# Performance work log

Hardware: AMD Instinct MI355X
Metric: run time of the kernel (lower is better)

## Reference

```python
import jax, jax.numpy as jnp
import numpy as np

N_NODES = 100000
N_EDGES = 1600000
N_FEAT = 128
HIDDEN = 64
N_CLASSES = 40


def setup_inputs() -> dict:
    key = jax.random.key(0)
    ks = jax.random.split(key, 4)
    x = jax.random.normal(ks[0], (N_NODES, N_FEAT), dtype=jnp.float32)
    edge_index = jax.random.randint(ks[1], (2, N_EDGES), 0, N_NODES, dtype=jnp.int64)
    # Glorot-style init like PyG GCNConv
    W1 = jax.random.normal(ks[2], (N_FEAT, HIDDEN), dtype=jnp.float32) * (1.0 / np.sqrt(N_FEAT))
    b1 = jnp.zeros((HIDDEN,), dtype=jnp.float32)
    W2 = jax.random.normal(ks[3], (HIDDEN, N_CLASSES), dtype=jnp.float32) * (1.0 / np.sqrt(HIDDEN))
    b2 = jnp.zeros((N_CLASSES,), dtype=jnp.float32)
    return {"x": x, "edge_index": edge_index, "W1": W1, "b1": b1, "W2": W2, "b2": b2}


def _gcn_conv(x, src, dst, norm, W, b, n_nodes):
    # PyG GCNConv: transform first, then normalized scatter-add aggregation
    h = x @ W                                   # [N, out]
    msg = h[src] * norm[:, None]                # [E+N, out] gather
    out = jax.ops.segment_sum(msg, dst, num_segments=n_nodes)  # scatter-add
    return out + b


def _norm_and_loops(edge_index, n_nodes):
    # add self-loops, symmetric normalization deg^{-1/2} A_hat deg^{-1/2}
    loop = jnp.arange(n_nodes, dtype=edge_index.dtype)
    src = jnp.concatenate([edge_index[0], loop])
    dst = jnp.concatenate([edge_index[1], loop])
    deg = jax.ops.segment_sum(jnp.ones_like(dst, dtype=jnp.float32), dst, num_segments=n_nodes)
    dinv = jnp.where(deg > 0, jax.lax.rsqrt(jnp.maximum(deg, 1.0)), 0.0)
    norm = dinv[src] * dinv[dst]
    return src, dst, norm


def reference(x, edge_index, W1, b1, W2, b2):
    n_nodes = x.shape[0]
    src, dst, norm = _norm_and_loops(edge_index, n_nodes)
    h = _gcn_conv(x, src, dst, norm, W1, b1, n_nodes)
    h = jax.nn.relu(h)
    h = _gcn_conv(h, src, dst, norm, W2, b2, n_nodes)
    return jax.nn.log_softmax(h, axis=1)
```

## Files before the change

### kernel.cpp

```cpp
#include <hip/hip_runtime.h>
#include <hip/hip_bf16.h>
#include <string.h>

#define N_FEAT 128
#define HIDDEN 64
#define N_CLS  40
#define EDGE_BLOCKS 1024
#define PLACE_BLOCKS 1024
#define PLACE_CHUNK 8192

typedef __bf16 bf16x8 __attribute__((ext_vector_type(8)));
typedef float  f32x4  __attribute__((ext_vector_type(4)));

union Frag { unsigned u[4]; bf16x8 v; };

static __device__ inline int get_xcc() {
    return (int)(__builtin_amdgcn_s_getreg((3 << 11) | 20) & 7u);
}


static __device__ inline unsigned pack_bf16(float a, float b) {
    unsigned ba = __float_as_uint(a);
    unsigned bb = __float_as_uint(b);
    unsigned ra = (ba + 0x7fffu + ((ba >> 16) & 1u)) >> 16;
    unsigned rb = (bb + 0x7fffu + ((bb >> 16) & 1u)) >> 16;
    return (ra & 0xffffu) | (rb << 16);
}

static __device__ inline float2 unpack_bf16(unsigned v) {
    return make_float2(__uint_as_float(v << 16), __uint_as_float(v & 0xffff0000u));
}


__global__ void detect_layout_kernel(const int* __restrict__ ei, int* __restrict__ flag) {
    int lane = threadIdx.x;
    int v = ei[2 * lane + 1];
    unsigned long long b = __ballot(v != 0);
    if (lane == 0) flag[0] = (b == 0ull) ? 1 : 0;
}


__global__ __launch_bounds__(256) void count_deg_kernel(const int* __restrict__ ei,
                                                        const int* __restrict__ flag,
                                                        unsigned* __restrict__ deg, int E) {
    bool is64 = (flag[0] != 0);
    int idx = blockIdx.x * 256 + threadIdx.x;
    if (is64) {
        int Eeven = E & ~1;
        int stride2 = gridDim.x * 256 * 2;
        for (int e = idx * 2; e < Eeven; e += stride2) {
            uint4 dv = *(const uint4*)(ei + (size_t)2 * E + (size_t)2 * e);
            atomicAdd(&deg[(int)dv.x], 1u);
            atomicAdd(&deg[(int)dv.z], 1u);
        }
        for (int e = Eeven + idx; e < E; e += gridDim.x * 256)
            atomicAdd(&deg[ei[(size_t)2 * E + (size_t)2 * e]], 1u);
    } else {
        for (int e = idx; e < E; e += gridDim.x * 256)
            atomicAdd(&deg[ei[(size_t)E + e]], 1u);
    }
}


__global__ __launch_bounds__(256) void scan_local_kernel(const unsigned* __restrict__ deg,
                                                         unsigned* __restrict__ rowptr,
                                                         float* __restrict__ dinv,
                                                         unsigned* __restrict__ partial, int N) {
    __shared__ unsigned tmp[256];
    int i = blockIdx.x * 256 + threadIdx.x;
    unsigned v = (i < N) ? deg[i] : 0u;
    if (i < N) dinv[i] = rsqrtf((float)(v + 1u));
    tmp[threadIdx.x] = v;
    __syncthreads();
#pragma unroll
    for (int off = 1; off < 256; off <<= 1) {
        unsigned t = (threadIdx.x >= (unsigned)off) ? tmp[threadIdx.x - off] : 0u;
        __syncthreads();
        tmp[threadIdx.x] += t;
        __syncthreads();
    }
    if (i < N) rowptr[i] = tmp[threadIdx.x] - v;
    if (threadIdx.x == 255) partial[blockIdx.x] = tmp[255];
}

__global__ __launch_bounds__(512) void scan_partial_kernel(unsigned* __restrict__ partial, int npart) {
    __shared__ unsigned tmp[512];
    unsigned v = ((int)threadIdx.x < npart) ? partial[threadIdx.x] : 0u;
    tmp[threadIdx.x] = v;
    __syncthreads();
#pragma unroll
    for (int off = 1; off < 512; off <<= 1) {
        unsigned t = (threadIdx.x >= (unsigned)off) ? tmp[threadIdx.x - off] : 0u;
        __syncthreads();
        tmp[threadIdx.x] += t;
        __syncthreads();
    }
    if ((int)threadIdx.x < npart) partial[threadIdx.x] = tmp[threadIdx.x] - v;
}

__global__ __launch_bounds__(256) void scan_add_kernel(unsigned* __restrict__ rowptr,
                                                       const unsigned* __restrict__ partial,
                                                       unsigned* __restrict__ cur, int N) {
    int i = blockIdx.x * 256 + threadIdx.x;
    if (i < N) {
        unsigned r = rowptr[i] + partial[blockIdx.x];
        rowptr[i] = r;
        cur[i] = r;
    }
}


__global__ __launch_bounds__(256) void place_xcd_kernel(const int* __restrict__ ei,
                                                        const int* __restrict__ flag,
                                                        unsigned* __restrict__ cur,
                                                        unsigned* __restrict__ ctr,
                                                        int* __restrict__ csr_src,
                                                        int E, int N) {
    int r = get_xcc();
    int npx = (N + 7) >> 3;
    int nlo = r * npx;
    int nhi = min(N, nlo + npx);
    bool is64 = (flag[0] != 0);
    __shared__ unsigned chunk_s;
    for (;;) {
        if (threadIdx.x == 0)
            chunk_s = __hip_atomic_fetch_add(&ctr[r * 64], 1u, __ATOMIC_RELAXED,
                                             __HIP_MEMORY_SCOPE_WORKGROUP);
        __syncthreads();
        long long base = (long long)chunk_s * PLACE_CHUNK;
        __syncthreads();
        if (base >= E) break;
        int end = (int)min((long long)E, base + PLACE_CHUNK);
        if (is64) {
            for (int e = (int)base + 2 * threadIdx.x; e + 1 < end; e += 512) {
                uint4 sv = *(const uint4*)(ei + (size_t)2 * e);
                uint4 dv = *(const uint4*)(ei + (size_t)2 * E + (size_t)2 * e);
                int d0 = (int)dv.x, d1 = (int)dv.z;
                if (d0 >= nlo && d0 < nhi) {
                    unsigned p = atomicAdd(&cur[d0], 1u);
                    csr_src[p] = (int)sv.x;
                }
                if (d1 >= nlo && d1 < nhi) {
                    unsigned p = atomicAdd(&cur[d1], 1u);
                    csr_src[p] = (int)sv.z;
                }
            }
            if ((end - (int)base) & 1) {
                if (threadIdx.x == 0) {
                    int e = end - 1;
                    int d = ei[(size_t)2 * E + (size_t)2 * e];
                    if (d >= nlo && d < nhi) {
                        unsigned p = atomicAdd(&cur[d], 1u);
                        csr_src[p] = ei[(size_t)2 * e];
                    }
                }
            }
        } else {
            for (int e = (int)base + threadIdx.x; e < end; e += 256) {
                int d = ei[(size_t)E + e];
                if (d >= nlo && d < nhi) {
                    unsigned p = atomicAdd(&cur[d], 1u);
                    csr_src[p] = ei[e];
                }
            }
        }
    }
}


__global__ __launch_bounds__(256) void gemm1_mfma_kernel(const float* __restrict__ x,
                                                         const float* __restrict__ W1,
                                                         unsigned* __restrict__ h1b, int N) {
    int lane = threadIdx.x & 63;
    int quad = lane >> 4;
    int col  = lane & 15;

    Frag B[4][4];
#pragma unroll
    for (int c = 0; c < 4; ++c)
#pragma unroll
        for (int ks = 0; ks < 4; ++ks) {
            int n = c * 16 + col;
#pragma unroll
            for (int jj = 0; jj < 4; ++jj) {
                int k = ks * 32 + quad * 8 + 2 * jj;
                B[c][ks].u[jj] = pack_bf16(W1[k * HIDDEN + n], W1[(k + 1) * HIDDEN + n]);
            }
        }

    int wave_id = blockIdx.x * 4 + (threadIdx.x >> 6);
    int nwaves  = gridDim.x * 4;
    int ntiles  = (N + 15) >> 4;

    for (int rt = wave_id; rt < ntiles; rt += nwaves) {
        int rowA = rt * 16 + col;
        Frag A[4];
#pragma unroll
        for (int ks = 0; ks < 4; ++ks) {
            float4 a0 = make_float4(0.f, 0.f, 0.f, 0.f), a1 = a0;
            if (rowA < N) {
                const float4* ap = (const float4*)(x + (size_t)rowA * N_FEAT + ks * 32 + quad * 8);
                a0 = ap[0];
                a1 = ap[1];
            }
            A[ks].u[0] = pack_bf16(a0.x, a0.y);
            A[ks].u[1] = pack_bf16(a0.z, a0.w);
            A[ks].u[2] = pack_bf16(a1.x, a1.y);
            A[ks].u[3] = pack_bf16(a1.z, a1.w);
        }
        f32x4 acc[4] = {{0.f, 0.f, 0.f, 0.f}, {0.f, 0.f, 0.f, 0.f},
                        {0.f, 0.f, 0.f, 0.f}, {0.f, 0.f, 0.f, 0.f}};
#pragma unroll
        for (int ks = 0; ks < 4; ++ks)
#pragma unroll
            for (int c = 0; c < 4; ++c)
                acc[c] = __builtin_amdgcn_mfma_f32_16x16x32_bf16(A[ks].v, B[c][ks].v, acc[c], 0, 0, 0);

        int rowD = rt * 16 + quad * 4;
#pragma unroll
        for (int c = 0; c < 4; ++c)
#pragma unroll
            for (int r = 0; r < 4; ++r) {
                float v = acc[c][r];
                float nxt = __shfl_down(v, 1);
                int row = rowD + r;
                if (((lane & 1) == 0) && row < N)
                    h1b[(size_t)row * 32 + ((c * 16 + col) >> 1)] = pack_bf16(v, nxt);
            }
    }
}


__global__ __launch_bounds__(256) void gemm2_mfma_kernel(const unsigned* __restrict__ actb,
                                                         const float* __restrict__ W2,
                                                         unsigned* __restrict__ h2b, int N) {
    int lane = threadIdx.x & 63;
    int quad = lane >> 4;
    int col  = lane & 15;

    Frag B[3][2];
#pragma unroll
    for (int c = 0; c < 3; ++c)
#pragma unroll
        for (int ks = 0; ks < 2; ++ks) {
            int n = c * 16 + col;
#pragma unroll
            for (int jj = 0; jj < 4; ++jj) {
                int k = ks * 32 + quad * 8 + 2 * jj;
                float w0 = (n < N_CLS) ? W2[k * N_CLS + n] : 0.f;
                float w1 = (n < N_CLS) ? W2[(k + 1) * N_CLS + n] : 0.f;
                B[c][ks].u[jj] = pack_bf16(w0, w1);
            }
        }

    int wave_id = blockIdx.x * 4 + (threadIdx.x >> 6);
    int nwaves  = gridDim.x * 4;
    int ntiles  = (N + 15) >> 4;

    for (int rt = wave_id; rt < ntiles; rt += nwaves) {
        int rowA = rt * 16 + col;
        Frag A[2];
#pragma unroll
        for (int ks = 0; ks < 2; ++ks) {
            uint4 u = make_uint4(0u, 0u, 0u, 0u);
            if (rowA < N)
                u = *(const uint4*)(actb + (size_t)rowA * 32 + ks * 16 + quad * 4);
            A[ks].u[0] = u.x; A[ks].u[1] = u.y; A[ks].u[2] = u.z; A[ks].u[3] = u.w;
        }
        f32x4 acc[3] = {{0.f, 0.f, 0.f, 0.f}, {0.f, 0.f, 0.f, 0.f}, {0.f, 0.f, 0.f, 0.f}};
#pragma unroll
        for (int ks = 0; ks < 2; ++ks)
#pragma unroll
            for (int c = 0; c < 3; ++c)
                acc[c] = __builtin_amdgcn_mfma_f32_16x16x32_bf16(A[ks].v, B[c][ks].v, acc[c], 0, 0, 0);

        int rowD = rt * 16 + quad * 4;
#pragma unroll
        for (int c = 0; c < 3; ++c)
#pragma unroll
            for (int r = 0; r < 4; ++r) {
                float v = acc[c][r];
                float nxt = __shfl_down(v, 1);
                int row = rowD + r;
                int pair = (c * 16 + col) >> 1;
                if (((lane & 1) == 0) && pair < 20 && row < N)
                    h2b[(size_t)row * 20 + pair] = pack_bf16(v, nxt);
            }
    }
}


__global__ __launch_bounds__(256) void agg1_kernel(const unsigned* __restrict__ h1b,
                                                   const int* __restrict__ csr_src,
                                                   const unsigned* __restrict__ rowptr,
                                                   const unsigned* __restrict__ deg,
                                                   const float* __restrict__ dinv,
                                                   const float* __restrict__ b1,
                                                   unsigned* __restrict__ actb, int N) {
    int wave = threadIdx.x >> 6, lane = threadIdx.x & 63;
    int sub = lane >> 5, j = lane & 31;
    int d = blockIdx.x * 4 + wave;
    if (d >= N) return;
    float dv = dinv[d];
    float acc0 = 0.f, acc1 = 0.f;
    if (sub == 0) {
        float2 v = unpack_bf16(h1b[(size_t)d * 32 + j]);
        acc0 = dv * v.x; acc1 = dv * v.y;
    }
    unsigned beg = rowptr[d];
    int len = (int)deg[d];
    int i = 0;
    for (; i + 8 <= len; i += 8) {
        int s0 = csr_src[beg + i + sub];
        int s1 = csr_src[beg + i + 2 + sub];
        int s2 = csr_src[beg + i + 4 + sub];
        int s3 = csr_src[beg + i + 6 + sub];
        float w0 = dinv[s0], w1 = dinv[s1], w2 = dinv[s2], w3 = dinv[s3];
        unsigned v0 = h1b[(size_t)s0 * 32 + j];
        unsigned v1 = h1b[(size_t)s1 * 32 + j];
        unsigned v2 = h1b[(size_t)s2 * 32 + j];
        unsigned v3 = h1b[(size_t)s3 * 32 + j];
        float2 a0 = unpack_bf16(v0), a1 = unpack_bf16(v1);
        float2 a2 = unpack_bf16(v2), a3 = unpack_bf16(v3);
        acc0 += w0 * a0.x + w1 * a1.x + w2 * a2.x + w3 * a3.x;
        acc1 += w0 * a0.y + w1 * a1.y + w2 * a2.y + w3 * a3.y;
    }
    for (; i + 4 <= len; i += 4) {
        int sA = csr_src[beg + i + sub];
        int sB = csr_src[beg + i + 2 + sub];
        float wA = dinv[sA], wB = dinv[sB];
        float2 a = unpack_bf16(h1b[(size_t)sA * 32 + j]);
        float2 b = unpack_bf16(h1b[(size_t)sB * 32 + j]);
        acc0 += wA * a.x + wB * b.x;
        acc1 += wA * a.y + wB * b.y;
    }
    for (; i < len; i += 2) {
        int e = i + sub;
        if (e < len) {
            int s = csr_src[beg + e];
            float w = dinv[s];
            float2 a = unpack_bf16(h1b[(size_t)s * 32 + j]);
            acc0 += w * a.x;
            acc1 += w * a.y;
        }
    }
    acc0 += __shfl_xor(acc0, 32);
    acc1 += __shfl_xor(acc1, 32);
    if (sub == 0) {
        float2 bb = ((const float2*)b1)[j];
        float r0 = fmaxf(acc0 * dv + bb.x, 0.f);
        float r1 = fmaxf(acc1 * dv + bb.y, 0.f);
        actb[(size_t)d * 32 + j] = pack_bf16(r0, r1);
    }
}


__global__ __launch_bounds__(256) void agg2_lsm_kernel(const unsigned* __restrict__ h2b,
                                                       const int* __restrict__ csr_src,
                                                       const unsigned* __restrict__ rowptr,
                                                       const unsigned* __restrict__ deg,
                                                       const float* __restrict__ dinv,
                                                       const float* __restrict__ b2,
                                                       float* __restrict__ out, int N) {
    int wave = threadIdx.x >> 6, lane = threadIdx.x & 63;
    int sub = lane >> 5, j = lane & 31;
    bool act = (j < 20);
    int d = blockIdx.x * 4 + wave;
    if (d >= N) return;
    float dv = dinv[d];
    float acc0 = 0.f, acc1 = 0.f;
    if (sub == 0 && act) {
        float2 v = unpack_bf16(h2b[(size_t)d * 20 + j]);
        acc0 = dv * v.x; acc1 = dv * v.y;
    }
    unsigned beg = rowptr[d];
    int len = (int)deg[d];
    int i = 0;
    for (; i + 8 <= len; i += 8) {
        int s0 = csr_src[beg + i + sub];
        int s1 = csr_src[beg + i + 2 + sub];
        int s2 = csr_src[beg + i + 4 + sub];
        int s3 = csr_src[beg + i + 6 + sub];
        float w0 = dinv[s0], w1 = dinv[s1], w2 = dinv[s2], w3 = dinv[s3];
        if (act) {
            float2 a0 = unpack_bf16(h2b[(size_t)s0 * 20 + j]);
            float2 a1 = unpack_bf16(h2b[(size_t)s1 * 20 + j]);
            float2 a2 = unpack_bf16(h2b[(size_t)s2 * 20 + j]);
            float2 a3 = unpack_bf16(h2b[(size_t)s3 * 20 + j]);
            acc0 += w0 * a0.x + w1 * a1.x + w2 * a2.x + w3 * a3.x;
            acc1 += w0 * a0.y + w1 * a1.y + w2 * a2.y + w3 * a3.y;
        }
    }
    for (; i + 4 <= len; i += 4) {
        int sA = csr_src[beg + i + sub];
        int sB = csr_src[beg + i + 2 + sub];
        float wA = dinv[sA], wB = dinv[sB];
        if (act) {
            float2 a = unpack_bf16(h2b[(size_t)sA * 20 + j]);
            float2 b = unpack_bf16(h2b[(size_t)sB * 20 + j]);
            acc0 += wA * a.x + wB * b.x;
            acc1 += wA * a.y + wB * b.y;
        }
    }
    for (; i < len; i += 2) {
        int e = i + sub;
        if (e < len && act) {
            int s = csr_src[beg + e];
            float w = dinv[s];
            float2 a = unpack_bf16(h2b[(size_t)s * 20 + j]);
            acc0 += w * a.x;
            acc1 += w * a.y;
        }
    }
    acc0 += __shfl_xor(acc0, 32);
    acc1 += __shfl_xor(acc1, 32);
    float v0 = -1e30f, v1 = -1e30f;
    if (act) {
        float2 bb = ((const float2*)b2)[j];
        v0 = acc0 * dv + bb.x;
        v1 = acc1 * dv + bb.y;
    }
    float m = fmaxf(v0, v1);
#pragma unroll
    for (int off = 32; off > 0; off >>= 1)
        m = fmaxf(m, __shfl_xor(m, off));
    float ex = (act && sub == 0) ? (expf(v0 - m) + expf(v1 - m)) : 0.f;
#pragma unroll
    for (int off = 32; off > 0; off >>= 1)
        ex += __shfl_xor(ex, off);
    float ls = logf(ex);
    if (act && sub == 0) {
        float2* orow = (float2*)(out + (size_t)d * N_CLS);
        orow[j] = make_float2(v0 - m - ls, v1 - m - ls);
    }
}


static inline size_t align_up(size_t x) { return (x + 255) & ~(size_t)255; }

extern "C" void kernel_launch(void* const* d_in, const int* in_sizes, int n_in,
                              void* d_out, int out_size, void* d_ws, size_t ws_size,
                              hipStream_t stream) {
    const float* x  = (const float*)d_in[0];
    const int*   ei = (const int*)d_in[1];
    const float* W1 = (const float*)d_in[2];
    const float* b1 = (const float*)d_in[3];
    const float* W2 = (const float*)d_in[4];
    const float* b2 = (const float*)d_in[5];

    int N = in_sizes[0] / N_FEAT;
    int E = in_sizes[1] / 2;
    int nblk = (N + 255) / 256;

    char* ws = (char*)d_ws;
    int*      flag    = (int*)ws;       ws += 256;
    unsigned* ctrs    = (unsigned*)ws;  ws += 4096;
    unsigned* deg     = (unsigned*)ws;  ws += align_up((size_t)N * 4);
    float*    dinv    = (float*)ws;     ws += align_up((size_t)N * 4);
    unsigned* rowptr  = (unsigned*)ws;  ws += align_up((size_t)N * 4);
    unsigned* cur     = (unsigned*)ws;  ws += align_up((size_t)N * 4);
    unsigned* partial = (unsigned*)ws;  ws += 2048;
    int*      csr_src = (int*)ws;       ws += align_up((size_t)E * 4);
    unsigned* h1b     = (unsigned*)ws;  ws += align_up((size_t)N * 32 * 4);
    unsigned* actb    = (unsigned*)ws;  ws += align_up((size_t)N * 32 * 4);
    unsigned* h2b     = (unsigned*)ws;  ws += align_up((size_t)N * 20 * 4);

    hipMemsetAsync(deg, 0, (size_t)N * 4, stream);
    hipMemsetAsync(ctrs, 0, 4096, stream);

    detect_layout_kernel<<<1, 64, 0, stream>>>(ei, flag);

    count_deg_kernel<<<EDGE_BLOCKS, 256, 0, stream>>>(ei, flag, deg, E);
    scan_local_kernel<<<nblk, 256, 0, stream>>>(deg, rowptr, dinv, partial, N);
    scan_partial_kernel<<<1, 512, 0, stream>>>(partial, nblk);
    scan_add_kernel<<<nblk, 256, 0, stream>>>(rowptr, partial, cur, N);
    place_xcd_kernel<<<PLACE_BLOCKS, 256, 0, stream>>>(ei, flag, cur, ctrs, csr_src, E, N);

    gemm1_mfma_kernel<<<512, 256, 0, stream>>>(x, W1, h1b, N);
    agg1_kernel<<<(N + 3) / 4, 256, 0, stream>>>(h1b, csr_src, rowptr, deg, dinv, b1, actb, N);

    gemm2_mfma_kernel<<<512, 256, 0, stream>>>(actb, W2, h2b, N);
    agg2_lsm_kernel<<<(N + 3) / 4, 256, 0, stream>>>(h2b, csr_src, rowptr, deg, dinv, b2, (float*)d_out, N);
}
```

Measured before the change: 385.6 us.

## Reorder layer 2 to aggregate before transform and fuse GEMM2 with log-softmax

Layer 2 now aggregates the 64-wide hidden activations over neighbours first, then applies W2, the bias and log-softmax in one per-node kernel using scalar FMAs. This removes the separate MFMA GEMM2 pass and the h2b intermediate. The cost is gathering 64-wide rows (128 B) per edge instead of 40-wide (80 B), plus a per-thread 64x40 FMA loop with register pressure and broadcast W2 loads. Non-temporal loads are also added for the edge-index reads in the CSR placement kernel.

After: 420.3 us. +9.0%, slower.

```diff
diff --git a/kernel.cpp b/kernel.cpp
--- a/kernel.cpp
+++ b/kernel.cpp
@@ -11,11 +11,16 @@
 
 typedef __bf16 bf16x8 __attribute__((ext_vector_type(8)));
 typedef float  f32x4  __attribute__((ext_vector_type(4)));
+typedef unsigned u32x4 __attribute__((ext_vector_type(4)));
 
 union Frag { unsigned u[4]; bf16x8 v; };
 
 static __device__ inline int get_xcc() {
     return (int)(__builtin_amdgcn_s_getreg((3 << 11) | 20) & 7u);
+}
+
+static __device__ inline u32x4 ntload4(const void* p) {
+    return __builtin_nontemporal_load((const u32x4*)p);
 }
 
 
@@ -133,16 +138,16 @@
         int end = (int)min((long long)E, base + PLACE_CHUNK);
         if (is64) {
             for (int e = (int)base + 2 * threadIdx.x; e + 1 < end; e += 512) {
-                uint4 sv = *(const uint4*)(ei + (size_t)2 * e);
-                uint4 dv = *(const uint4*)(ei + (size_t)2 * E + (size_t)2 * e);
-                int d0 = (int)dv.x, d1 = (int)dv.z;
+                u32x4 sv = ntload4(ei + (size_t)2 * e);
+                u32x4 dv = ntload4(ei + (size_t)2 * E + (size_t)2 * e);
+                int d0 = (int)dv[0], d1 = (int)dv[2];
                 if (d0 >= nlo && d0 < nhi) {
                     unsigned p = atomicAdd(&cur[d0], 1u);
-                    csr_src[p] = (int)sv.x;
+                    csr_src[p] = (int)sv[0];
                 }
                 if (d1 >= nlo && d1 < nhi) {
                     unsigned p = atomicAdd(&cur[d1], 1u);
-                    csr_src[p] = (int)sv.z;
+                    csr_src[p] = (int)sv[2];
                 }
             }
             if ((end - (int)base) & 1) {
@@ -157,10 +162,11 @@
             }
         } else {
             for (int e = (int)base + threadIdx.x; e < end; e += 256) {
-                int d = ei[(size_t)E + e];
+                int d = __builtin_nontemporal_load(ei + (size_t)E + e);
                 if (d >= nlo && d < nhi) {
+                    int s = __builtin_nontemporal_load(ei + e);
                     unsigned p = atomicAdd(&cur[d], 1u);
-                    csr_src[p] = ei[e];
+                    csr_src[p] = s;
                 }
             }
         }
@@ -226,65 +232,6 @@
                 int row = rowD + r;
                 if (((lane & 1) == 0) && row < N)
                     h1b[(size_t)row * 32 + ((c * 16 + col) >> 1)] = pack_bf16(v, nxt);
-            }
-    }
-}
-
-
-__global__ __launch_bounds__(256) void gemm2_mfma_kernel(const unsigned* __restrict__ actb,
-                                                         const float* __restrict__ W2,
-                                                         unsigned* __restrict__ h2b, int N) {
-    int lane = threadIdx.x & 63;
-    int quad = lane >> 4;
-    int col  = lane & 15;
-
-    Frag B[3][2];
-#pragma unroll
-    for (int c = 0; c < 3; ++c)
-#pragma unroll
-        for (int ks = 0; ks < 2; ++ks) {
-            int n = c * 16 + col;
-#pragma unroll
-            for (int jj = 0; jj < 4; ++jj) {
-                int k = ks * 32 + quad * 8 + 2 * jj;
-                float w0 = (n < N_CLS) ? W2[k * N_CLS + n] : 0.f;
-                float w1 = (n < N_CLS) ? W2[(k + 1) * N_CLS + n] : 0.f;
-                B[c][ks].u[jj] = pack_bf16(w0, w1);
-            }
-        }
-
-    int wave_id = blockIdx.x * 4 + (threadIdx.x >> 6);
-    int nwaves  = gridDim.x * 4;
-    int ntiles  = (N + 15) >> 4;
-
-    for (int rt = wave_id; rt < ntiles; rt += nwaves) {
-        int rowA = rt * 16 + col;
-        Frag A[2];
-#pragma unroll
-        for (int ks = 0; ks < 2; ++ks) {
-            uint4 u = make_uint4(0u, 0u, 0u, 0u);
-            if (rowA < N)
-                u = *(const uint4*)(actb + (size_t)rowA * 32 + ks * 16 + quad * 4);
-            A[ks].u[0] = u.x; A[ks].u[1] = u.y; A[ks].u[2] = u.z; A[ks].u[3] = u.w;
-        }
-        f32x4 acc[3] = {{0.f, 0.f, 0.f, 0.f}, {0.f, 0.f, 0.f, 0.f}, {0.f, 0.f, 0.f, 0.f}};
-#pragma unroll
-        for (int ks = 0; ks < 2; ++ks)
-#pragma unroll
-            for (int c = 0; c < 3; ++c)
-                acc[c] = __builtin_amdgcn_mfma_f32_16x16x32_bf16(A[ks].v, B[c][ks].v, acc[c], 0, 0, 0);
-
-        int rowD = rt * 16 + quad * 4;
-#pragma unroll
-        for (int c = 0; c < 3; ++c)
-#pragma unroll
-            for (int r = 0; r < 4; ++r) {
-                float v = acc[c][r];
-                float nxt = __shfl_down(v, 1);
-                int row = rowD + r;
-                int pair = (c * 16 + col) >> 1;
-                if (((lane & 1) == 0) && pair < 20 && row < N)
-                    h2b[(size_t)row * 20 + pair] = pack_bf16(v, nxt);
             }
     }
 }
@@ -355,22 +302,20 @@
 }
 
 
-__global__ __launch_bounds__(256) void agg2_lsm_kernel(const unsigned* __restrict__ h2b,
-                                                       const int* __restrict__ csr_src,
-                                                       const unsigned* __restrict__ rowptr,
-                                                       const unsigned* __restrict__ deg,
-                                                       const float* __restrict__ dinv,
-                                                       const float* __restrict__ b2,
-                                                       float* __restrict__ out, int N) {
+__global__ __launch_bounds__(256) void agg2g_kernel(const unsigned* __restrict__ actb,
+                                                    const int* __restrict__ csr_src,
+                                                    const unsigned* __restrict__ rowptr,
+                                                    const unsigned* __restrict__ deg,
+                                                    const float* __restrict__ dinv,
+                                                    unsigned* __restrict__ gb, int N) {
     int wave = threadIdx.x >> 6, lane = threadIdx.x & 63;
     int sub = lane >> 5, j = lane & 31;
-    bool act = (j < 20);
     int d = blockIdx.x * 4 + wave;
     if (d >= N) return;
     float dv = dinv[d];
     float acc0 = 0.f, acc1 = 0.f;
-    if (sub == 0 && act) {
-        float2 v = unpack_bf16(h2b[(size_t)d * 20 + j]);
+    if (sub == 0) {
+        float2 v = unpack_bf16(actb[(size_t)d * 32 + j]);
         acc0 = dv * v.x; acc1 = dv * v.y;
     }
     unsigned beg = rowptr[d];
@@ -382,56 +327,80 @@
         int s2 = csr_src[beg + i + 4 + sub];
         int s3 = csr_src[beg + i + 6 + sub];
         float w0 = dinv[s0], w1 = dinv[s1], w2 = dinv[s2], w3 = dinv[s3];
-        if (act) {
-            float2 a0 = unpack_bf16(h2b[(size_t)s0 * 20 + j]);
-            float2 a1 = unpack_bf16(h2b[(size_t)s1 * 20 + j]);
-            float2 a2 = unpack_bf16(h2b[(size_t)s2 * 20 + j]);
-            float2 a3 = unpack_bf16(h2b[(size_t)s3 * 20 + j]);
-            acc0 += w0 * a0.x + w1 * a1.x + w2 * a2.x + w3 * a3.x;
-            acc1 += w0 * a0.y + w1 * a1.y + w2 * a2.y + w3 * a3.y;
-        }
+        unsigned v0 = actb[(size_t)s0 * 32 + j];
+        unsigned v1 = actb[(size_t)s1 * 32 + j];
+        unsigned v2 = actb[(size_t)s2 * 32 + j];
+        unsigned v3 = actb[(size_t)s3 * 32 + j];
+        float2 a0 = unpack_bf16(v0), a1 = unpack_bf16(v1);
+        float2 a2 = unpack_bf16(v2), a3 = unpack_bf16(v3);
+        acc0 += w0 * a0.x + w1 * a1.x + w2 * a2.x + w3 * a3.x;
+        acc1 += w0 * a0.y + w1 * a1.y + w2 * a2.y + w3 * a3.y;
     }
     for (; i + 4 <= len; i += 4) {
         int sA = csr_src[beg + i + sub];
         int sB = csr_src[beg + i + 2 + sub];
         float wA = dinv[sA], wB = dinv[sB];
-        if (act) {
-            float2 a = unpack_bf16(h2b[(size_t)sA * 20 + j]);
-            float2 b = unpack_bf16(h2b[(size_t)sB * 20 + j]);
-            acc0 += wA * a.x + wB * b.x;
-            acc1 += wA * a.y + wB * b.y;
-        }
+        float2 a = unpack_bf16(actb[(size_t)sA * 32 + j]);
+        float2 b = unpack_bf16(actb[(size_t)sB * 32 + j]);
+        acc0 += wA * a.x + wB * b.x;
+        acc1 += wA * a.y + wB * b.y;
     }
     for (; i < len; i += 2) {
         int e = i + sub;
-        if (e < len && act) {
+        if (e < len) {
             int s = csr_src[beg + e];
             float w = dinv[s];
-            float2 a = unpack_bf16(h2b[(size_t)s * 20 + j]);
+            float2 a = unpack_bf16(actb[(size_t)s * 32 + j]);
             acc0 += w * a.x;
             acc1 += w * a.y;
         }
     }
     acc0 += __shfl_xor(acc0, 32);
     acc1 += __shfl_xor(acc1, 32);
-    float v0 = -1e30f, v1 = -1e30f;
-    if (act) {
-        float2 bb = ((const float2*)b2)[j];
-        v0 = acc0 * dv + bb.x;
-        v1 = acc1 * dv + bb.y;
-    }
-    float m = fmaxf(v0, v1);
-#pragma unroll
-    for (int off = 32; off > 0; off >>= 1)
-        m = fmaxf(m, __shfl_xor(m, off));
-    float ex = (act && sub == 0) ? (expf(v0 - m) + expf(v1 - m)) : 0.f;
-#pragma unroll
-    for (int off = 32; off > 0; off >>= 1)
-        ex += __shfl_xor(ex, off);
-    float ls = logf(ex);
-    if (act && sub == 0) {
-        float2* orow = (float2*)(out + (size_t)d * N_CLS);
-        orow[j] = make_float2(v0 - m - ls, v1 - m - ls);
+    if (sub == 0)
+        gb[(size_t)d * 32 + j] = pack_bf16(acc0 * dv, acc1 * dv);
+}
+
+
+__global__ __launch_bounds__(256) void gemm2lsm_kernel(const unsigned* __restrict__ gb,
+                                                       const float* __restrict__ W2,
+                                                       const float* __restrict__ b2,
+                                                       float* __restrict__ out, int N) {
+    int d = blockIdx.x * 256 + threadIdx.x;
+    if (d >= N) return;
+    float z[N_CLS];
+#pragma unroll
+    for (int c = 0; c < N_CLS; ++c) z[c] = b2[c];
+
+    const uint4* gp = (const uint4*)(gb + (size_t)d * 32);
+#pragma unroll
+    for (int p = 0; p < 8; ++p) {
+        uint4 u = gp[p];
+        float2 f0 = unpack_bf16(u.x), f1 = unpack_bf16(u.y);
+        float2 f2 = unpack_bf16(u.z), f3 = unpack_bf16(u.w);
+        float f[8] = {f0.x, f0.y, f1.x, f1.y, f2.x, f2.y, f3.x, f3.y};
+#pragma unroll
+        for (int q = 0; q < 8; ++q) {
+            int k = p * 8 + q;
+#pragma unroll
+            for (int c = 0; c < N_CLS; ++c)
+                z[c] = fmaf(f[q], W2[k * N_CLS + c], z[c]);
+        }
+    }
+    float m = z[0];
+#pragma unroll
+    for (int c = 1; c < N_CLS; ++c) m = fmaxf(m, z[c]);
+    float s = 0.f;
+#pragma unroll
+    for (int c = 0; c < N_CLS; ++c) s += __expf(z[c] - m);
+    float ls = __logf(s) + m;
+    float4* orow = (float4*)(out + (size_t)d * N_CLS);
+#pragma unroll
+    for (int q = 0; q < 10; ++q) {
+        float4 o;
+        o.x = z[q * 4 + 0] - ls; o.y = z[q * 4 + 1] - ls;
+        o.z = z[q * 4 + 2] - ls; o.w = z[q * 4 + 3] - ls;
+        orow[q] = o;
     }
 }
 
@@ -463,7 +432,7 @@
     int*      csr_src = (int*)ws;       ws += align_up((size_t)E * 4);
     unsigned* h1b     = (unsigned*)ws;  ws += align_up((size_t)N * 32 * 4);
     unsigned* actb    = (unsigned*)ws;  ws += align_up((size_t)N * 32 * 4);
-    unsigned* h2b     = (unsigned*)ws;  ws += align_up((size_t)N * 20 * 4);
+    unsigned* gb      = (unsigned*)ws;  ws += align_up((size_t)N * 32 * 4);
 
     hipMemsetAsync(deg, 0, (size_t)N * 4, stream);
     hipMemsetAsync(ctrs, 0, 4096, stream);
@@ -479,6 +448,6 @@
     gemm1_mfma_kernel<<<512, 256, 0, stream>>>(x, W1, h1b, N);
     agg1_kernel<<<(N + 3) / 4, 256, 0, stream>>>(h1b, csr_src, rowptr, deg, dinv, b1, actb, N);
 
-    gemm2_mfma_kernel<<<512, 256, 0, stream>>>(actb, W2, h2b, N);
-    agg2_lsm_kernel<<<(N + 3) / 4, 256, 0, stream>>>(h2b, csr_src, rowptr, deg, dinv, b2, (float*)d_out, N);
-}
+    agg2g_kernel<<<(N + 3) / 4, 256, 0, stream>>>(actb, csr_src, rowptr, deg, dinv, gb, N);
+    gemm2lsm_kernel<<<nblk, 256, 0, stream>>>(gb, W2, b2, (float*)d_out, N);
+}
```
